# Optimization experiments

Measured on AMD Instinct MI355X. Metric: run time of the kernel, lower is better.

## Reference

```python
import jax, jax.numpy as jnp
import numpy as np

B = 4096          # walker batch
S0, S1 = 8, 8     # up / down spins
N = S0 + S1       # total electrons
M = 4             # nucleons
D = 16            # determinants
N_ONE = [256, 256, 256, 256]
N_TWO = [32, 32, 32, 32]


def setup_inputs() -> dict:
    key = jax.random.key(0)
    ks = jax.random.split(key, 16)
    f0 = 8 + 3 * 4 * M              # 56, first-layer one-stream input
    f1 = 3 * N_ONE[0] + 2 * N_TWO[0]  # 832, later-layer one-stream input
    s = 0.05
    return {
        "x": jax.random.normal(ks[0], (B, N, 3), jnp.float32),
        "nucleon_pos": jnp.asarray([[0.0, 0.0, 0.0], [0.0, 0.0, 1.4],
                                    [1.2, 0.0, 0.0], [0.0, 1.2, 0.7]], jnp.float32),
        "v0_w": s * jax.random.normal(ks[1], (N_ONE[0], f0), jnp.float32),
        "v0_b": s * jax.random.normal(ks[2], (N_ONE[0],), jnp.float32),
        "v_w": s * jax.random.normal(ks[3], (3, N_ONE[0], f1), jnp.float32),
        "v_b": s * jax.random.normal(ks[4], (3, N_ONE[0]), jnp.float32),
        "w0_w": s * jax.random.normal(ks[5], (N_TWO[0], 4), jnp.float32),
        "w0_b": s * jax.random.normal(ks[6], (N_TWO[0],), jnp.float32),
        "w_w": s * jax.random.normal(ks[7], (3, N_TWO[0], N_TWO[0]), jnp.float32),
        "w_b": s * jax.random.normal(ks[8], (3, N_TWO[0]), jnp.float32),
        "env_w": s * jax.random.normal(ks[9], (D, N, N_ONE[-1]), jnp.float32),
        "env_g": jax.random.uniform(ks[10], (D, N), jnp.float32),
        "sigma": jax.random.uniform(ks[11], (D, N, M), jnp.float32),
        "pi": jax.random.uniform(ks[12], (D, N, M), jnp.float32),
    }


def _safe_norm(v, axis):
    # ||v||_2 with a zero (not NaN) gradient at v == 0 (diagonal e-e distances).
    s = jnp.sum(v * v, axis=axis)
    return jnp.sqrt(jnp.where(s == 0, 1.0, s)) * (s > 0)


def reference(x, nucleon_pos, v0_w, v0_b, v_w, v_b, w0_w, w0_b, w_w, w_b,
              env_w, env_g, sigma, pi):
    b = x.shape[0]
    # electron-electron stream: [B,N,N,4], [b,i,j] = x_j - x_i, |x_j - x_i|
    tev = x[:, None, :, :] - x[:, :, None, :]
    two = jnp.concatenate([tev, _safe_norm(tev, -1)[..., None]], axis=-1)
    # electron-nucleus: oev[b,m,n] = x_n - R_m  -> [B,M,N,3]
    oev = x[:, None, :, :] - nucleon_pos[:, None, :]
    oed = jnp.linalg.norm(oev, axis=-1)                     # [B,M,N]
    one = jnp.concatenate([oev, oed[..., None]], axis=-1)   # [B,M,N,4]
    one = jnp.transpose(one, (0, 2, 1, 3)).reshape(b, N, 4 * M)  # [B,N,4M]
    oev_p = jnp.transpose(oev, (0, 2, 1, 3))                # [B,N,M,3]

    for l in range(len(N_ONE)):
        g1u = jnp.mean(one[:, :S0], axis=1)                 # [B,F]
        g1d = jnp.mean(one[:, S0:], axis=1)
        g2u = jnp.mean(two[:, :, :S0, :], axis=2)           # [B,N,F2]
        g2d = jnp.mean(two[:, :, S0:, :], axis=2)
        f = jnp.concatenate([
            one,
            jnp.broadcast_to(g1u[:, None], (b, N, g1u.shape[-1])),
            jnp.broadcast_to(g1d[:, None], (b, N, g1d.shape[-1])),
            g2u, g2d], axis=-1)
        Wv, bv = (v0_w, v0_b) if l == 0 else (v_w[l - 1], v_b[l - 1])
        Ww, bw = (w0_w, w0_b) if l == 0 else (w_w[l - 1], w_b[l - 1])
        new_one = jnp.tanh(jnp.einsum('bnf,of->bno', f, Wv) + bv)
        new_two = jnp.tanh(jnp.einsum('bijf,of->bijo', two, Ww) + bw)
        if l > 0 and N_ONE[l] == N_ONE[l - 1] and N_TWO[l] == N_TWO[l - 1]:
            new_one = new_one + one
            new_two = new_two + two
        one, two = new_one, new_two

    r = jnp.linalg.norm(oev_p, axis=-1)                     # [B,N,M]
    F = N_ONE[-1]

    def block(rows, cols):
        ew = env_w[:, rows]                # [D,ni,F]
        eg = env_g[:, rows]                # [D,ni]
        sg = jnp.abs(sigma[:, rows])       # [D,ni,M]
        pw = pi[:, rows]                   # [D,ni,M]
        h = one[:, cols]                   # [B,nj,F]
        rj = r[:, cols]                    # [B,nj,M]
        # sum_f (w*h + g) = w.h + F*g
        lin = jnp.einsum('kif,bjf->bkij', ew, h) + F * eg[None, :, :, None]
        env = jnp.zeros(lin.shape, lin.dtype)
        for m in range(M):                 # small static loop over nucleons
            env = env + pw[None, :, :, None, m] * jnp.exp(
                -sg[None, :, :, None, m] * rj[:, None, None, :, m])
        return lin * env                   # [B,D,ni,nj]

    psi_up = block(slice(0, S0), slice(0, S0))
    psi_dn = block(slice(0, S1), slice(S0, N))  # original reuses row params k*N+i
    d = jnp.linalg.det(psi_up) * jnp.linalg.det(psi_dn)     # [B,D]
    return jnp.sum(d, axis=1)                               # [B]
```

## Files before the change

kernel.cpp:

```cpp
#include <hip/hip_runtime.h>
#include <cmath>

namespace {

typedef unsigned short u16;
typedef unsigned int u32;
using short8  = __attribute__((ext_vector_type(8))) short;
using float4v = __attribute__((ext_vector_type(4))) float;

constexpr size_t MB_HI   = 0;
constexpr size_t MB_LO   = 638976;
constexpr size_t L0_HI   = 1277952;
constexpr size_t L0_LO   = L0_HI + 16384;
constexpr size_t ENV_HI  = L0_LO + 16384;
constexpr size_t ENV_LO  = ENV_HI + 32768;
constexpr size_t TWOB_HI = ENV_LO + 32768;
constexpr size_t TWOB_LO = TWOB_HI + 4096;

__device__ __forceinline__ u16 f2bf(float f) {
    u32 u = __float_as_uint(f);
    u += 0x7FFFu + ((u >> 16) & 1u);
    return (u16)(u >> 16);
}
__device__ __forceinline__ float bf2f(u16 h) {
    return __uint_as_float(((u32)h) << 16);
}
__device__ __forceinline__ float fast_tanh(float x) {
    float e = __expf(-2.f * fabsf(x));
    float t = (1.f - e) * __builtin_amdgcn_rcpf(1.f + e);
    return copysignf(t, x);
}

__global__ void k_prep_main(const float* __restrict__ vw, u16* __restrict__ hi, u16* __restrict__ lo) {
    int id = blockIdx.x * 256 + threadIdx.x;
    int l = id / 212992, rem = id % 212992;
    int ks = rem >> 13;
    int r2 = rem & 8191;
    int nt = r2 >> 9, lane = (r2 >> 3) & 63, j = r2 & 7;
    int n = nt * 16 + (lane & 15);
    int f = ks * 32 + ((lane >> 4) << 3) + j;
    float w = vw[(size_t)(l * 256 + n) * 832 + f];
    u16 h = f2bf(w);
    hi[id] = h; lo[id] = f2bf(w - bf2f(h));
}
__global__ void k_prep_l0(const float* __restrict__ v0w, u16* __restrict__ hi, u16* __restrict__ lo) {
    int id = blockIdx.x * 256 + threadIdx.x;
    int ks = id >> 13;
    int r2 = id & 8191;
    int nt = r2 >> 9, lane = (r2 >> 3) & 63, j = r2 & 7;
    int n = nt * 16 + (lane & 15);
    int f = ks * 32 + ((lane >> 4) << 3) + j;
    float w = (f < 56) ? v0w[n * 56 + f] : 0.f;
    u16 h = f2bf(w);
    hi[id] = h; lo[id] = f2bf(w - bf2f(h));
}
__global__ void k_prep_env(const float* __restrict__ ew, u16* __restrict__ hi, u16* __restrict__ lo) {
    int id = blockIdx.x * 256 + threadIdx.x;
    int ks = id >> 12;
    int r2 = id & 4095;
    int nt = r2 >> 9, lane = (r2 >> 3) & 63, j = r2 & 7;
    int n = nt * 16 + (lane & 15);
    int f = ks * 32 + ((lane >> 4) << 3) + j;
    float w = ew[(size_t)(((n >> 3) * 16) + (n & 7)) * 256 + f];
    u16 h = f2bf(w);
    hi[id] = h; lo[id] = f2bf(w - bf2f(h));
}
__global__ void k_prep_two(const float* __restrict__ w0w, const float* __restrict__ ww,
                           u16* __restrict__ hi, u16* __restrict__ lo) {
    int id = blockIdx.x * 256 + threadIdx.x;
    int l = id >> 10, r = id & 1023;
    int nt = r >> 9, lane = (r >> 3) & 63, j = r & 7;
    int n = nt * 16 + (lane & 15);
    int f = ((lane >> 4) << 3) + j;
    float w;
    if (l == 0) w = (f < 4) ? w0w[n * 4 + f] : 0.f;
    else        w = ww[(size_t)(((l - 1) * 32) + n) * 32 + f];
    u16 h = f2bf(w);
    hi[id] = h; lo[id] = f2bf(w - bf2f(h));
}

template <bool L0, bool RES, bool LAST>
__device__ __forceinline__ void layer_run(
    int t, float (&prev)[4][4],
    u16 (*stateF)[32][16][8], u16 (*twoF)[16][4][16][8],
    u16 (*g2F)[8][16][8], u16 (*g1F)[2][8][4][8],
    const u16* __restrict__ Bhi, const u16* __restrict__ Blo,
    const u16* __restrict__ TBhi, const u16* __restrict__ TBlo,
    const float* __restrict__ bvp, const float* __restrict__ bwp)
{
    const int lane = t & 63, wv = t >> 6, quad = lane >> 4, l16 = lane & 15;
    float4v acc[4];
    #pragma unroll
    for (int q = 0; q < 4; ++q) acc[q] = (float4v){0.f, 0.f, 0.f, 0.f};

    const size_t wb0 = (size_t)(wv * 4) * 512 + (size_t)lane * 8;

    auto mfma_step = [&](int ks, short8 Ah, short8 Al) {
        const u16* bh = Bhi + wb0 + (size_t)ks * 8192;
        const u16* bl = Blo + wb0 + (size_t)ks * 8192;
        #pragma unroll
        for (int q = 0; q < 4; ++q) {
            short8 Wh = *(const short8*)(bh + q * 512);
            short8 Wl = *(const short8*)(bl + q * 512);
            acc[q] = __builtin_amdgcn_mfma_f32_16x16x32_bf16(Ah, Wh, acc[q], 0, 0, 0);
            acc[q] = __builtin_amdgcn_mfma_f32_16x16x32_bf16(Al, Wh, acc[q], 0, 0, 0);
            acc[q] = __builtin_amdgcn_mfma_f32_16x16x32_bf16(Ah, Wl, acc[q], 0, 0, 0);
        }
    };

    if (L0) {
        #pragma unroll
        for (int ks = 0; ks < 2; ++ks) {
            short8 Ah = *(const short8*)&g2F[0][ks * 4 + quad][l16][0];
            short8 Al = *(const short8*)&g2F[1][ks * 4 + quad][l16][0];
            mfma_step(ks, Ah, Al);
        }
    } else {
        #pragma unroll 2
        for (int ks = 0; ks < 8; ++ks) {
            short8 Ah = *(const short8*)&stateF[0][ks * 4 + quad][l16][0];
            short8 Al = *(const short8*)&stateF[1][ks * 4 + quad][l16][0];
            mfma_step(ks, Ah, Al);
        }
        #pragma unroll 4
        for (int ks = 8; ks < 24; ++ks) {
            const int ud = (ks < 16) ? 0 : 1;
            const int kg = (ks - 8) & 7;
            short8 Ah = *(const short8*)&g1F[0][ud][kg][quad][0];
            short8 Al = *(const short8*)&g1F[1][ud][kg][quad][0];
            mfma_step(ks, Ah, Al);
        }
        #pragma unroll
        for (int ks = 24; ks < 26; ++ks) {
            short8 Ah = *(const short8*)&g2F[0][(ks - 24) * 4 + quad][l16][0];
            short8 Al = *(const short8*)&g2F[1][(ks - 24) * 4 + quad][l16][0];
            mfma_step(ks, Ah, Al);
        }
    }

    float4v tac[4][2];
    #pragma unroll
    for (int mt = 0; mt < 4; ++mt)
        #pragma unroll
        for (int nt = 0; nt < 2; ++nt) tac[mt][nt] = (float4v){0.f, 0.f, 0.f, 0.f};
    {
        short8 TWh[2], TWl[2];
        #pragma unroll
        for (int nt = 0; nt < 2; ++nt) {
            TWh[nt] = *(const short8*)(TBhi + nt * 512 + (size_t)lane * 8);
            TWl[nt] = *(const short8*)(TBlo + nt * 512 + (size_t)lane * 8);
        }
        #pragma unroll
        for (int mt = 0; mt < 4; ++mt) {
            const int it = wv * 4 + mt;
            short8 Ah = *(const short8*)&twoF[0][it][quad][l16][0];
            short8 Al = *(const short8*)&twoF[1][it][quad][l16][0];
            #pragma unroll
            for (int nt = 0; nt < 2; ++nt) {
                tac[mt][nt] = __builtin_amdgcn_mfma_f32_16x16x32_bf16(Ah, TWh[nt], tac[mt][nt], 0, 0, 0);
                tac[mt][nt] = __builtin_amdgcn_mfma_f32_16x16x32_bf16(Al, TWh[nt], tac[mt][nt], 0, 0, 0);
                tac[mt][nt] = __builtin_amdgcn_mfma_f32_16x16x32_bf16(Ah, TWl[nt], tac[mt][nt], 0, 0, 0);
            }
        }
    }
    __syncthreads();

    #pragma unroll
    for (int q = 0; q < 4; ++q) {
        const int n = (wv * 4 + q) * 16 + l16;
        const float bvv = bvp[n];
        #pragma unroll
        for (int r = 0; r < 4; ++r) {
            float v = fast_tanh(acc[q][r] + bvv);
            if (RES) v += prev[q][r];
            prev[q][r] = v;
        }
        if (!LAST) {
            float su = 0.f, sd = 0.f;
            #pragma unroll
            for (int r = 0; r < 4; ++r) { if (quad < 2) su += prev[q][r]; else sd += prev[q][r]; }
            su += __shfl_xor(su, 16); su += __shfl_xor(su, 32);
            sd += __shfl_xor(sd, 16); sd += __shfl_xor(sd, 32);
            if (quad == 0) {
                const int kg = n >> 5, qd = (n >> 3) & 3, jj = n & 7;
                float mu = su * 0.125f, md = sd * 0.125f;
                u16 hu = f2bf(mu), hd = f2bf(md);
                g1F[0][0][kg][qd][jj] = hu; g1F[1][0][kg][qd][jj] = f2bf(mu - bf2f(hu));
                g1F[0][1][kg][qd][jj] = hd; g1F[1][1][kg][qd][jj] = f2bf(md - bf2f(hd));
            }
        }
        const int ko = n >> 3, jj = n & 7;
        #pragma unroll
        for (int r = 0; r < 4; ++r) {
            const int m = quad * 4 + r;
            u16 h = f2bf(prev[q][r]);
            stateF[0][ko][m][jj] = h;
            stateF[1][ko][m][jj] = f2bf(prev[q][r] - bf2f(h));
        }
    }

    if (!LAST) {
        #pragma unroll
        for (int mt = 0; mt < 4; ++mt) {
            const int it = wv * 4 + mt;
            float tv[2][4];
            #pragma unroll
            for (int nt = 0; nt < 2; ++nt) {
                const int c = nt * 16 + l16;
                const float bwv = bwp[c];
                #pragma unroll
                for (int r = 0; r < 4; ++r) {
                    float v = fast_tanh(tac[mt][nt][r] + bwv);
                    if (RES) {
                        const int j = quad * 4 + r;
                        v += bf2f(twoF[0][it][c >> 3][j][c & 7])
                           + bf2f(twoF[1][it][c >> 3][j][c & 7]);
                    }
                    tv[nt][r] = v;
                }
            }
            #pragma unroll
            for (int nt = 0; nt < 2; ++nt) {
                float s = tv[nt][0] + tv[nt][1] + tv[nt][2] + tv[nt][3];
                float su = (quad < 2) ? s : 0.f;
                float sd = (quad >= 2) ? s : 0.f;
                su += __shfl_xor(su, 16); su += __shfl_xor(su, 32);
                sd += __shfl_xor(sd, 16); sd += __shfl_xor(sd, 32);
                if (quad == 0) {
                    const int c = nt * 16 + l16;
                    float mu = su * 0.125f, md = sd * 0.125f;
                    u16 hu = f2bf(mu), hd = f2bf(md);
                    g2F[0][c >> 3][it][c & 7] = hu;
                    g2F[1][c >> 3][it][c & 7] = f2bf(mu - bf2f(hu));
                    g2F[0][4 + (c >> 3)][it][c & 7] = hd;
                    g2F[1][4 + (c >> 3)][it][c & 7] = f2bf(md - bf2f(hd));
                }
            }
            #pragma unroll
            for (int nt = 0; nt < 2; ++nt) {
                const int c = nt * 16 + l16;
                #pragma unroll
                for (int r = 0; r < 4; ++r) {
                    const int j = quad * 4 + r;
                    u16 h = f2bf(tv[nt][r]);
                    twoF[0][it][c >> 3][j][c & 7] = h;
                    twoF[1][it][c >> 3][j][c & 7] = f2bf(tv[nt][r] - bf2f(h));
                }
            }
        }
    }
    __syncthreads();
}

__global__ __launch_bounds__(256, 2) void ferminet_kernel(
    const float* __restrict__ x,
    const float* __restrict__ nuc,
    const float* __restrict__ v0_b,
    const float* __restrict__ v_b,
    const float* __restrict__ w0_b,
    const float* __restrict__ w_b,
    const float* __restrict__ env_g,
    const float* __restrict__ sigma,
    const float* __restrict__ pi_,
    const u16* __restrict__ wsB,
    float* __restrict__ out)
{
    __shared__ u16  stateF[2][32][16][8];
    __shared__ u16  twoF[2][16][4][16][8];
    __shared__ u16  g2F[2][8][16][8];
    __shared__ u16  g1F[2][2][8][4][8];
    __shared__ float xs[48];
    __shared__ float rs[64];
    __shared__ float dets[2][16];
    float* psi = (float*)&stateF[0][0][0][0];

    const int t = threadIdx.x;
    const int b = blockIdx.x;
    const int lane = t & 63, wv = t >> 6, quad = lane >> 4, l16 = lane & 15;

    if (t < 48) xs[t] = x[(size_t)b * 48 + t];
    if (t >= 128 && t < 192) ((u32*)&g2F[0][7][0][0])[t - 128] = 0u;
    if (t >= 192 && t < 256) ((u32*)&g2F[1][7][0][0])[t - 192] = 0u;
    __syncthreads();

    if (t < 64) {
        int n = t >> 2, m = t & 3;
        float ox = xs[n * 3 + 0] - nuc[m * 3 + 0];
        float oy = xs[n * 3 + 1] - nuc[m * 3 + 1];
        float oz = xs[n * 3 + 2] - nuc[m * 3 + 2];
        float d = sqrtf(ox * ox + oy * oy + oz * oz);
        rs[n * 4 + m] = d;
        float v[4] = {ox, oy, oz, d};
        #pragma unroll
        for (int c = 0; c < 4; ++c) {
            int k = m * 4 + c;
            u16 h = f2bf(v[c]);
            g2F[0][k >> 3][n][k & 7] = h;
            g2F[1][k >> 3][n][k & 7] = f2bf(v[c] - bf2f(h));
        }
        #pragma unroll
        for (int c = 0; c < 4; ++c) {
            float s = v[c];
            s += __shfl_xor(s, 4); s += __shfl_xor(s, 8); s += __shfl_xor(s, 16);
            if ((n & 7) == 0) {
                float mn = s * 0.125f;
                int k = 16 + (n >> 3) * 16 + m * 4 + c;
                u16 h = f2bf(mn);
                u16 lo = f2bf(mn - bf2f(h));
                #pragma unroll
                for (int mm = 0; mm < 16; ++mm) {
                    g2F[0][k >> 3][mm][k & 7] = h;
                    g2F[1][k >> 3][mm][k & 7] = lo;
                }
            }
        }
    }
    {
        int i = t >> 4, j = t & 15;
        float dx = xs[j * 3 + 0] - xs[i * 3 + 0];
        float dy = xs[j * 3 + 1] - xs[i * 3 + 1];
        float dz = xs[j * 3 + 2] - xs[i * 3 + 2];
        float s2 = dx * dx + dy * dy + dz * dz;
        float nr = (s2 > 0.f) ? sqrtf(s2) : 0.f;
        float tv[4] = {dx, dy, dz, nr};
        short8 z = {0, 0, 0, 0, 0, 0, 0, 0};
        #pragma unroll
        for (int p = 0; p < 2; ++p)
            #pragma unroll
            for (int ko = 0; ko < 4; ++ko) *(short8*)&twoF[p][i][ko][j][0] = z;
        #pragma unroll
        for (int c = 0; c < 4; ++c) {
            u16 h = f2bf(tv[c]);
            twoF[0][i][0][j][c] = h;
            twoF[1][i][0][j][c] = f2bf(tv[c] - bf2f(h));
        }
        #pragma unroll
        for (int c = 0; c < 4; ++c) {
            float v = tv[c];
            v += __shfl_xor(v, 1); v += __shfl_xor(v, 2); v += __shfl_xor(v, 4);
            if ((t & 7) == 0) {
                float mn = v * 0.125f;
                int k = 48 + ((t >> 3) & 1) * 4 + c;
                u16 h = f2bf(mn);
                g2F[0][k >> 3][i][k & 7] = h;
                g2F[1][k >> 3][i][k & 7] = f2bf(mn - bf2f(h));
            }
        }
    }
    __syncthreads();

    float prev[4][4];
    layer_run<true,  false, false>(t, prev, stateF, twoF, g2F, g1F,
        wsB + L0_HI, wsB + L0_LO, wsB + TWOB_HI, wsB + TWOB_LO, v0_b, w0_b);
    layer_run<false, true,  false>(t, prev, stateF, twoF, g2F, g1F,
        wsB + MB_HI + 0 * 212992, wsB + MB_LO + 0 * 212992,
        wsB + TWOB_HI + 1024, wsB + TWOB_LO + 1024, v_b + 0 * 256, w_b + 0 * 32);
    layer_run<false, true,  false>(t, prev, stateF, twoF, g2F, g1F,
        wsB + MB_HI + 1 * 212992, wsB + MB_LO + 1 * 212992,
        wsB + TWOB_HI + 2048, wsB + TWOB_LO + 2048, v_b + 1 * 256, w_b + 1 * 32);
    layer_run<false, true,  true >(t, prev, stateF, twoF, g2F, g1F,
        wsB + MB_HI + 2 * 212992, wsB + MB_LO + 2 * 212992,
        wsB + TWOB_HI + 3072, wsB + TWOB_LO + 3072, v_b + 2 * 256, w_b + 2 * 32);

    {
        float4v ac2[2];
        ac2[0] = (float4v){0.f, 0.f, 0.f, 0.f};
        ac2[1] = (float4v){0.f, 0.f, 0.f, 0.f};
        const size_t wb0 = (size_t)(wv * 2) * 512 + (size_t)lane * 8;
        const u16* Eh = wsB + ENV_HI;
        const u16* El = wsB + ENV_LO;
        #pragma unroll 2
        for (int ks = 0; ks < 8; ++ks) {
            short8 Ah = *(const short8*)&stateF[0][ks * 4 + quad][l16][0];
            short8 Al = *(const short8*)&stateF[1][ks * 4 + quad][l16][0];
            const u16* bh = Eh + wb0 + (size_t)ks * 4096;
            const u16* bl = El + wb0 + (size_t)ks * 4096;
            #pragma unroll
            for (int q = 0; q < 2; ++q) {
                short8 Wh = *(const short8*)(bh + q * 512);
                short8 Wl = *(const short8*)(bl + q * 512);
                ac2[q] = __builtin_amdgcn_mfma_f32_16x16x32_bf16(Ah, Wh, ac2[q], 0, 0, 0);
                ac2[q] = __builtin_amdgcn_mfma_f32_16x16x32_bf16(Al, Wh, ac2[q], 0, 0, 0);
                ac2[q] = __builtin_amdgcn_mfma_f32_16x16x32_bf16(Ah, Wl, ac2[q], 0, 0, 0);
            }
        }
        float vals[2][4];
        int kk[2], ii[2];
        #pragma unroll
        for (int q = 0; q < 2; ++q) {
            const int n = (wv * 2 + q) * 16 + l16;
            const int k = n >> 3, i = n & 7, kif = k * 16 + i;
            kk[q] = k; ii[q] = i;
            const float lc = 256.f * env_g[kif];
            const float4 pw4 = *(const float4*)&pi_[(size_t)kif * 4];
            const float4 sg4 = *(const float4*)&sigma[(size_t)kif * 4];
            const float sg[4] = {fabsf(sg4.x), fabsf(sg4.y), fabsf(sg4.z), fabsf(sg4.w)};
            const float pw[4] = {pw4.x, pw4.y, pw4.z, pw4.w};
            #pragma unroll
            for (int r = 0; r < 4; ++r) {
                const int je = quad * 4 + r;
                float E = 0.f;
                #pragma unroll
                for (int m = 0; m < 4; ++m) E += pw[m] * __expf(-sg[m] * rs[je * 4 + m]);
                vals[q][r] = (ac2[q][r] + lc) * E;
            }
        }
        __syncthreads();
        #pragma unroll
        for (int q = 0; q < 2; ++q) {
            #pragma unroll
            for (int r = 0; r < 4; ++r) {
                const int je = quad * 4 + r;
                const int s = je >> 3, j = je & 7;
                psi[((s * 16 + kk[q]) * 8 + ii[q]) * 8 + j] = vals[q][r];
            }
        }
    }
    __syncthreads();

    if (t < 32) {
        int s = t >> 4, k = t & 15;
        const float* src = psi + (s * 16 + k) * 64;
        float m[8][8];
        #pragma unroll
        for (int i = 0; i < 8; ++i)
            #pragma unroll
            for (int j = 0; j < 8; ++j) m[i][j] = src[i * 8 + j];
        float det = 1.f;
        #pragma unroll
        for (int c = 0; c < 8; ++c) {
            #pragma unroll
            for (int r = c + 1; r < 8; ++r) {
                if (fabsf(m[r][c]) > fabsf(m[c][c])) {
                    det = -det;
                    #pragma unroll
                    for (int j = 0; j < 8; ++j) {
                        float tmp = m[c][j]; m[c][j] = m[r][j]; m[r][j] = tmp;
                    }
                }
            }
            float piv = m[c][c];
            det *= piv;
            if (piv != 0.f) {
                float inv = 1.f / piv;
                #pragma unroll
                for (int r = c + 1; r < 8; ++r) {
                    float fac = m[r][c] * inv;
                    #pragma unroll
                    for (int j = c; j < 8; ++j) m[r][j] -= fac * m[c][j];
                }
            }
        }
        dets[s][k] = det;
    }
    __syncthreads();

    if (t == 0) {
        float s = 0.f;
        #pragma unroll
        for (int k = 0; k < 16; ++k) s += dets[0][k] * dets[1][k];
        out[b] = s;
    }
}

}

extern "C" void kernel_launch(void* const* d_in, const int* in_sizes, int n_in,
                              void* d_out, int out_size, void* d_ws, size_t ws_size,
                              hipStream_t stream) {
    (void)n_in; (void)out_size; (void)ws_size;
    const float* x    = (const float*)d_in[0];
    const float* nuc  = (const float*)d_in[1];
    const float* v0w  = (const float*)d_in[2];
    const float* v0b  = (const float*)d_in[3];
    const float* vw   = (const float*)d_in[4];
    const float* vb   = (const float*)d_in[5];
    const float* w0w  = (const float*)d_in[6];
    const float* w0b  = (const float*)d_in[7];
    const float* ww   = (const float*)d_in[8];
    const float* wb   = (const float*)d_in[9];
    const float* envw = (const float*)d_in[10];
    const float* envg = (const float*)d_in[11];
    const float* sig  = (const float*)d_in[12];
    const float* pii  = (const float*)d_in[13];
    float* out = (float*)d_out;
    u16* wsB = (u16*)d_ws;

    k_prep_main<<<638976 / 256, 256, 0, stream>>>(vw, wsB + MB_HI, wsB + MB_LO);
    k_prep_l0  <<<16384 / 256, 256, 0, stream>>>(v0w, wsB + L0_HI, wsB + L0_LO);
    k_prep_env <<<32768 / 256, 256, 0, stream>>>(envw, wsB + ENV_HI, wsB + ENV_LO);
    k_prep_two <<<4096 / 256, 256, 0, stream>>>(w0w, ww, wsB + TWOB_HI, wsB + TWOB_LO);

    const int B = in_sizes[0] / 48;
    ferminet_kernel<<<B, 256, 0, stream>>>(x, nuc, v0b, vb, w0b, wb,
                                           envg, sig, pii, wsB, out);
}
```

Measured before the change: 569.6 us.

## Keep two-stream state in registers as MFMA fragments, shrink LDS, raise occupancy

The two-electron stream state is now held in per-wave register fragments (twoA) laid out as MFMA A operands, replacing the 32KB shared twoF array. Each wave transposes its tanh outputs through a small per-wave scratch buffer (twoS) to rebuild the fragments and to compute the up/down means with in-lane shuffles. The initial two-stream means are computed directly from positions. The smaller LDS footprint lets launch bounds rise from 2 to 4 blocks per CU, at the cost of more register pressure and possible spills.

Measured after the change: 715.9 us. +25.7%, slower.

```diff
diff --git a/kernel.cpp b/kernel.cpp
--- a/kernel.cpp
+++ b/kernel.cpp
@@ -81,9 +81,9 @@
 
 template <bool L0, bool RES, bool LAST>
 __device__ __forceinline__ void layer_run(
-    int t, float (&prev)[4][4],
-    u16 (*stateF)[32][16][8], u16 (*twoF)[16][4][16][8],
-    u16 (*g2F)[8][16][8], u16 (*g1F)[2][8][4][8],
+    int t, float (&prev)[4][4], short8 (&twoA)[2][4],
+    u16 (*stateF)[32][16][8], u16 (*g2F)[8][16][8], u16 (*g1F)[2][8][4][8],
+    float (*twoS)[36],
     const u16* __restrict__ Bhi, const u16* __restrict__ Blo,
     const u16* __restrict__ TBhi, const u16* __restrict__ TBlo,
     const float* __restrict__ bvp, const float* __restrict__ bwp)
@@ -144,22 +144,15 @@
         #pragma unroll
         for (int nt = 0; nt < 2; ++nt) tac[mt][nt] = (float4v){0.f, 0.f, 0.f, 0.f};
     {
-        short8 TWh[2], TWl[2];
         #pragma unroll
         for (int nt = 0; nt < 2; ++nt) {
-            TWh[nt] = *(const short8*)(TBhi + nt * 512 + (size_t)lane * 8);
-            TWl[nt] = *(const short8*)(TBlo + nt * 512 + (size_t)lane * 8);
-        }
-        #pragma unroll
-        for (int mt = 0; mt < 4; ++mt) {
-            const int it = wv * 4 + mt;
-            short8 Ah = *(const short8*)&twoF[0][it][quad][l16][0];
-            short8 Al = *(const short8*)&twoF[1][it][quad][l16][0];
-            #pragma unroll
-            for (int nt = 0; nt < 2; ++nt) {
-                tac[mt][nt] = __builtin_amdgcn_mfma_f32_16x16x32_bf16(Ah, TWh[nt], tac[mt][nt], 0, 0, 0);
-                tac[mt][nt] = __builtin_amdgcn_mfma_f32_16x16x32_bf16(Al, TWh[nt], tac[mt][nt], 0, 0, 0);
-                tac[mt][nt] = __builtin_amdgcn_mfma_f32_16x16x32_bf16(Ah, TWl[nt], tac[mt][nt], 0, 0, 0);
+            short8 TWh = *(const short8*)(TBhi + nt * 512 + (size_t)lane * 8);
+            short8 TWl = *(const short8*)(TBlo + nt * 512 + (size_t)lane * 8);
+            #pragma unroll
+            for (int mt = 0; mt < 4; ++mt) {
+                tac[mt][nt] = __builtin_amdgcn_mfma_f32_16x16x32_bf16(twoA[0][mt], TWh, tac[mt][nt], 0, 0, 0);
+                tac[mt][nt] = __builtin_amdgcn_mfma_f32_16x16x32_bf16(twoA[1][mt], TWh, tac[mt][nt], 0, 0, 0);
+                tac[mt][nt] = __builtin_amdgcn_mfma_f32_16x16x32_bf16(twoA[0][mt], TWl, tac[mt][nt], 0, 0, 0);
             }
         }
     }
@@ -203,56 +196,47 @@
         #pragma unroll
         for (int mt = 0; mt < 4; ++mt) {
             const int it = wv * 4 + mt;
-            float tv[2][4];
             #pragma unroll
             for (int nt = 0; nt < 2; ++nt) {
                 const int c = nt * 16 + l16;
                 const float bwv = bwp[c];
                 #pragma unroll
-                for (int r = 0; r < 4; ++r) {
-                    float v = fast_tanh(tac[mt][nt][r] + bwv);
-                    if (RES) {
-                        const int j = quad * 4 + r;
-                        v += bf2f(twoF[0][it][c >> 3][j][c & 7])
-                           + bf2f(twoF[1][it][c >> 3][j][c & 7]);
-                    }
-                    tv[nt][r] = v;
+                for (int r = 0; r < 4; ++r)
+                    twoS[quad * 4 + r][c] = fast_tanh(tac[mt][nt][r] + bwv);
+            }
+            float4 ra = *(const float4*)&twoS[l16][quad * 8];
+            float4 rb = *(const float4*)&twoS[l16][quad * 8 + 4];
+            float nv[8] = {ra.x, ra.y, ra.z, ra.w, rb.x, rb.y, rb.z, rb.w};
+            #pragma unroll
+            for (int j2 = 0; j2 < 8; ++j2) {
+                float v = nv[j2];
+                if (RES) v += bf2f((u16)twoA[0][mt][j2]) + bf2f((u16)twoA[1][mt][j2]);
+                nv[j2] = v;
+                u16 h = f2bf(v);
+                twoA[0][mt][j2] = (short)h;
+                twoA[1][mt][j2] = (short)f2bf(v - bf2f(h));
+            }
+            #pragma unroll
+            for (int j2 = 0; j2 < 8; ++j2) {
+                float s = nv[j2];
+                s += __shfl_xor(s, 1); s += __shfl_xor(s, 2); s += __shfl_xor(s, 4);
+                nv[j2] = s * 0.125f;
+            }
+            if (l16 == 0 || l16 == 8) {
+                const int base = (l16 == 0) ? 0 : 4;
+                #pragma unroll
+                for (int j2 = 0; j2 < 8; ++j2) {
+                    u16 h = f2bf(nv[j2]);
+                    g2F[0][base + quad][it][j2] = h;
+                    g2F[1][base + quad][it][j2] = f2bf(nv[j2] - bf2f(h));
                 }
             }
-            #pragma unroll
-            for (int nt = 0; nt < 2; ++nt) {
-                float s = tv[nt][0] + tv[nt][1] + tv[nt][2] + tv[nt][3];
-                float su = (quad < 2) ? s : 0.f;
-                float sd = (quad >= 2) ? s : 0.f;
-                su += __shfl_xor(su, 16); su += __shfl_xor(su, 32);
-                sd += __shfl_xor(sd, 16); sd += __shfl_xor(sd, 32);
-                if (quad == 0) {
-                    const int c = nt * 16 + l16;
-                    float mu = su * 0.125f, md = sd * 0.125f;
-                    u16 hu = f2bf(mu), hd = f2bf(md);
-                    g2F[0][c >> 3][it][c & 7] = hu;
-                    g2F[1][c >> 3][it][c & 7] = f2bf(mu - bf2f(hu));
-                    g2F[0][4 + (c >> 3)][it][c & 7] = hd;
-                    g2F[1][4 + (c >> 3)][it][c & 7] = f2bf(md - bf2f(hd));
-                }
-            }
-            #pragma unroll
-            for (int nt = 0; nt < 2; ++nt) {
-                const int c = nt * 16 + l16;
-                #pragma unroll
-                for (int r = 0; r < 4; ++r) {
-                    const int j = quad * 4 + r;
-                    u16 h = f2bf(tv[nt][r]);
-                    twoF[0][it][c >> 3][j][c & 7] = h;
-                    twoF[1][it][c >> 3][j][c & 7] = f2bf(tv[nt][r] - bf2f(h));
-                }
-            }
-        }
-    }
-    __syncthreads();
-}
-
-__global__ __launch_bounds__(256, 2) void ferminet_kernel(
+        }
+    }
+    __syncthreads();
+}
+
+__global__ __launch_bounds__(256, 4) void ferminet_kernel(
     const float* __restrict__ x,
     const float* __restrict__ nuc,
     const float* __restrict__ v0_b,
@@ -266,9 +250,9 @@
     float* __restrict__ out)
 {
     __shared__ u16  stateF[2][32][16][8];
-    __shared__ u16  twoF[2][16][4][16][8];
     __shared__ u16  g2F[2][8][16][8];
     __shared__ u16  g1F[2][2][8][4][8];
+    __shared__ float twoS[4][16][36];
     __shared__ float xs[48];
     __shared__ float rs[64];
     __shared__ float dets[2][16];
@@ -315,50 +299,64 @@
             }
         }
     }
+    if (t < 128) {
+        int i = t >> 3, ud = (t >> 2) & 1, c = t & 3;
+        float s = 0.f;
+        #pragma unroll
+        for (int jo = 0; jo < 8; ++jo) {
+            int j = ud * 8 + jo;
+            float dx = xs[j * 3 + 0] - xs[i * 3 + 0];
+            float dy = xs[j * 3 + 1] - xs[i * 3 + 1];
+            float dz = xs[j * 3 + 2] - xs[i * 3 + 2];
+            float v;
+            if (c == 0) v = dx;
+            else if (c == 1) v = dy;
+            else if (c == 2) v = dz;
+            else { float s2 = dx * dx + dy * dy + dz * dz; v = (s2 > 0.f) ? sqrtf(s2) : 0.f; }
+            s += v;
+        }
+        float mn = s * 0.125f;
+        int k = 48 + ud * 4 + c;
+        u16 h = f2bf(mn);
+        g2F[0][6][i][k & 7] = h;
+        g2F[1][6][i][k & 7] = f2bf(mn - bf2f(h));
+    }
+    short8 twoA[2][4];
     {
-        int i = t >> 4, j = t & 15;
-        float dx = xs[j * 3 + 0] - xs[i * 3 + 0];
-        float dy = xs[j * 3 + 1] - xs[i * 3 + 1];
-        float dz = xs[j * 3 + 2] - xs[i * 3 + 2];
-        float s2 = dx * dx + dy * dy + dz * dz;
-        float nr = (s2 > 0.f) ? sqrtf(s2) : 0.f;
-        float tv[4] = {dx, dy, dz, nr};
-        short8 z = {0, 0, 0, 0, 0, 0, 0, 0};
-        #pragma unroll
-        for (int p = 0; p < 2; ++p)
-            #pragma unroll
-            for (int ko = 0; ko < 4; ++ko) *(short8*)&twoF[p][i][ko][j][0] = z;
-        #pragma unroll
-        for (int c = 0; c < 4; ++c) {
-            u16 h = f2bf(tv[c]);
-            twoF[0][i][0][j][c] = h;
-            twoF[1][i][0][j][c] = f2bf(tv[c] - bf2f(h));
-        }
-        #pragma unroll
-        for (int c = 0; c < 4; ++c) {
-            float v = tv[c];
-            v += __shfl_xor(v, 1); v += __shfl_xor(v, 2); v += __shfl_xor(v, 4);
-            if ((t & 7) == 0) {
-                float mn = v * 0.125f;
-                int k = 48 + ((t >> 3) & 1) * 4 + c;
-                u16 h = f2bf(mn);
-                g2F[0][k >> 3][i][k & 7] = h;
-                g2F[1][k >> 3][i][k & 7] = f2bf(mn - bf2f(h));
+        short8 z8 = {0, 0, 0, 0, 0, 0, 0, 0};
+        #pragma unroll
+        for (int mt = 0; mt < 4; ++mt) { twoA[0][mt] = z8; twoA[1][mt] = z8; }
+        if (quad == 0) {
+            #pragma unroll
+            for (int mt = 0; mt < 4; ++mt) {
+                const int it = wv * 4 + mt;
+                float dx = xs[l16 * 3 + 0] - xs[it * 3 + 0];
+                float dy = xs[l16 * 3 + 1] - xs[it * 3 + 1];
+                float dz = xs[l16 * 3 + 2] - xs[it * 3 + 2];
+                float s2 = dx * dx + dy * dy + dz * dz;
+                float nr = (s2 > 0.f) ? sqrtf(s2) : 0.f;
+                float v[4] = {dx, dy, dz, nr};
+                #pragma unroll
+                for (int c = 0; c < 4; ++c) {
+                    u16 h = f2bf(v[c]);
+                    twoA[0][mt][c] = (short)h;
+                    twoA[1][mt][c] = (short)f2bf(v[c] - bf2f(h));
+                }
             }
         }
     }
     __syncthreads();
 
     float prev[4][4];
-    layer_run<true,  false, false>(t, prev, stateF, twoF, g2F, g1F,
+    layer_run<true,  false, false>(t, prev, twoA, stateF, g2F, g1F, twoS[wv],
         wsB + L0_HI, wsB + L0_LO, wsB + TWOB_HI, wsB + TWOB_LO, v0_b, w0_b);
-    layer_run<false, true,  false>(t, prev, stateF, twoF, g2F, g1F,
+    layer_run<false, true,  false>(t, prev, twoA, stateF, g2F, g1F, twoS[wv],
         wsB + MB_HI + 0 * 212992, wsB + MB_LO + 0 * 212992,
         wsB + TWOB_HI + 1024, wsB + TWOB_LO + 1024, v_b + 0 * 256, w_b + 0 * 32);
-    layer_run<false, true,  false>(t, prev, stateF, twoF, g2F, g1F,
+    layer_run<false, true,  false>(t, prev, twoA, stateF, g2F, g1F, twoS[wv],
         wsB + MB_HI + 1 * 212992, wsB + MB_LO + 1 * 212992,
         wsB + TWOB_HI + 2048, wsB + TWOB_LO + 2048, v_b + 1 * 256, w_b + 1 * 32);
-    layer_run<false, true,  true >(t, prev, stateF, twoF, g2F, g1F,
+    layer_run<false, true,  true >(t, prev, twoA, stateF, g2F, g1F, twoS[wv],
         wsB + MB_HI + 2 * 212992, wsB + MB_LO + 2 * 212992,
         wsB + TWOB_HI + 3072, wsB + TWOB_LO + 3072, v_b + 2 * 256, w_b + 2 * 32);
 
```
